# Kernel optimization log

Measured on AMD Instinct MI355X. Metric: run time of the kernel, lower is better.

Reference implementation:

```python
import jax, jax.numpy as jnp
import numpy as np

EPS = 1e-12  # F.normalize default eps


def setup_inputs() -> dict:
    key = jax.random.key(0)
    ks = jax.random.split(key, 6)
    B, C, D, H, W = 8, 192, 24, 24, 24
    heads = 6
    x = jax.random.normal(ks[0], (B, C, D, H, W), dtype=jnp.float32)
    qkv_w = jax.random.normal(ks[1], (3 * C, C), dtype=jnp.float32) * (1.0 / np.sqrt(C))
    qkv_b = jax.random.normal(ks[2], (3 * C,), dtype=jnp.float32) * 0.02
    temperature = jnp.ones((heads, 1, 1), dtype=jnp.float32)
    proj_w = jax.random.normal(ks[3], (C, C), dtype=jnp.float32) * (1.0 / np.sqrt(C))
    proj_b = jax.random.normal(ks[4], (C,), dtype=jnp.float32) * 0.02
    return {"x": x, "qkv_w": qkv_w, "qkv_b": qkv_b, "temperature": temperature,
            "proj_w": proj_w, "proj_b": proj_b}


def _l2norm_lastdim(t):
    n = jnp.sqrt(jnp.sum(t * t, axis=-1, keepdims=True))
    return t / jnp.maximum(n, EPS)


def reference(x, qkv_w, qkv_b, temperature, proj_w, proj_b):
    B, C, D, H, W = x.shape
    N = D * H * W
    heads = temperature.shape[0]
    hd = C // heads
    xf = x.reshape(B, C, N)
    # 1x1x1 Conv3d == per-voxel linear over channels: (B, 3C, N)
    qkv = jnp.einsum('bcn,oc->bon', xf, qkv_w) + qkv_b[None, :, None]
    # Faithful torch reshape of contiguous (B, 3C, N) buffer -> (B, N, 3, heads, hd),
    # then permute(2,0,3,4,1) -> (3, B, heads, hd, N)
    qkv = qkv.reshape(B, N, 3, heads, hd).transpose(2, 0, 3, 4, 1)
    q, k, v = qkv[0], qkv[1], qkv[2]
    q = _l2norm_lastdim(q)
    k = _l2norm_lastdim(k)
    # channel cross-covariance attention: (B, heads, hd, hd)
    attn = jnp.einsum('bhcn,bhdn->bhcd', q, k) * temperature[None]
    attn = jax.nn.softmax(attn, axis=-1)
    out = jnp.einsum('bhcd,bhdn->bhcn', attn, v)          # (B, heads, hd, N)
    out = out.transpose(0, 2, 1, 3).reshape(B, C, D, H, W)  # transpose(1,2) + reshape
    outf = out.reshape(B, C, N)
    y = jnp.einsum('bcn,oc->bon', outf, proj_w) + proj_b[None, :, None]
    return y.reshape(B, C, D, H, W)
```

## Files before the change

kernel.cpp:

```cpp
#include <hip/hip_runtime.h>

#define B_ 8
#define C_ 192
#define N_ 13824
#define HEADS 6
#define HD 32
#define THREEC 576
#define CH 54

typedef unsigned short ushort_t;
typedef unsigned int uint_t;
typedef __attribute__((ext_vector_type(8))) short short8;
typedef __attribute__((ext_vector_type(4))) float f32x4;

__device__ __forceinline__ float bf2f(ushort_t u) {
  union { uint_t u; float f; } c; c.u = ((uint_t)u) << 16; return c.f;
}
__device__ __forceinline__ float lo_f(uint_t u) {
  union { uint_t u; float f; } c; c.u = u << 16; return c.f;
}
__device__ __forceinline__ float hi_f(uint_t u) {
  union { uint_t u; float f; } c; c.u = u & 0xffff0000u; return c.f;
}
__device__ __forceinline__ ushort_t f2bf(float f) {
  union { float f; uint_t u; } c; c.f = f;
  uint_t u = c.u;
  uint_t r = (u + 0x7fffu + ((u >> 16) & 1u)) >> 16;
  return (ushort_t)r;
}

#define LROW 200

__global__ __launch_bounds__(256, 2) void qkv_fused(
    const float* __restrict__ x, const float* __restrict__ w,
    const float* __restrict__ bias, ushort_t* __restrict__ qkv) {
  __shared__ ushort_t Bs[128 * LROW];
  __shared__ ushort_t As[64 * LROW];
  int t = threadIdx.x;
  int n0 = blockIdx.x * 128, b = blockIdx.y;
  int wid = t >> 6, lane = t & 63;
  int ln16 = lane & 15, q4 = lane >> 4;
  const float* xb = x + (size_t)b * C_ * N_;

  {
    int nl = t & 127;
    int cb0 = (t >> 7) * 8;
#pragma unroll
    for (int it = 0; it < 12; ++it) {
      int cb = cb0 + it * 16;
      float v[8];
#pragma unroll
      for (int j = 0; j < 8; ++j)
        v[j] = xb[(size_t)(cb + j) * N_ + n0 + nl];
      union { ushort_t us[8]; uint4 u4; } pk;
#pragma unroll
      for (int j = 0; j < 8; ++j) pk.us[j] = f2bf(v[j]);
      *(uint4*)&Bs[nl * LROW + cb] = pk.u4;
    }
  }

  int ar = t >> 2, au0 = t & 3;
  uint4 apre[6];
#pragma unroll
  for (int j = 0; j < 6; ++j) {
    int u = au0 + 4 * j;
    const float* src = w + (size_t)ar * C_ + u * 8;
    float4 v0 = *(const float4*)src;
    float4 v1 = *(const float4*)(src + 4);
    union { ushort_t us[8]; uint4 u4; } pk;
    pk.us[0] = f2bf(v0.x); pk.us[1] = f2bf(v0.y); pk.us[2] = f2bf(v0.z); pk.us[3] = f2bf(v0.w);
    pk.us[4] = f2bf(v1.x); pk.us[5] = f2bf(v1.y); pk.us[6] = f2bf(v1.z); pk.us[7] = f2bf(v1.w);
    apre[j] = pk.u4;
  }

  __syncthreads();

#pragma unroll
  for (int j = 0; j < 6; ++j)
    *(uint4*)&As[ar * LROW + (au0 + 4 * j) * 8] = apre[j];

  int ncol = (wid & 1) * 64, mrow = (wid >> 1) * 32;
  short8 bb[6][4];
#pragma unroll
  for (int kk = 0; kk < 6; ++kk)
#pragma unroll
    for (int ni = 0; ni < 4; ++ni)
      bb[kk][ni] = *(const short8*)&Bs[(ncol + ni * 16 + ln16) * LROW + kk * 32 + q4 * 8];

  __syncthreads();

  for (int p = 0; p < 9; ++p) {
    if (p < 8) {
      int o0n = (p + 1) * 64;
#pragma unroll
      for (int j = 0; j < 6; ++j) {
        int u = au0 + 4 * j;
        const float* src = w + (size_t)(o0n + ar) * C_ + u * 8;
        float4 v0 = *(const float4*)src;
        float4 v1 = *(const float4*)(src + 4);
        union { ushort_t us[8]; uint4 u4; } pk;
        pk.us[0] = f2bf(v0.x); pk.us[1] = f2bf(v0.y); pk.us[2] = f2bf(v0.z); pk.us[3] = f2bf(v0.w);
        pk.us[4] = f2bf(v1.x); pk.us[5] = f2bf(v1.y); pk.us[6] = f2bf(v1.z); pk.us[7] = f2bf(v1.w);
        apre[j] = pk.u4;
      }
    }

    float brg[2][4];
#pragma unroll
    for (int mi = 0; mi < 2; ++mi)
#pragma unroll
      for (int r = 0; r < 4; ++r)
        brg[mi][r] = bias[p * 64 + mrow + mi * 16 + q4 * 4 + r];

    f32x4 acc[2][4];
#pragma unroll
    for (int mi = 0; mi < 2; ++mi)
#pragma unroll
      for (int ni = 0; ni < 4; ++ni) acc[mi][ni] = (f32x4){0.f, 0.f, 0.f, 0.f};

#pragma unroll
    for (int kk = 0; kk < 6; ++kk) {
      short8 a[2];
#pragma unroll
      for (int mi = 0; mi < 2; ++mi)
        a[mi] = *(const short8*)&As[(mrow + mi * 16 + ln16) * LROW + kk * 32 + q4 * 8];
#pragma unroll
      for (int mi = 0; mi < 2; ++mi)
#pragma unroll
        for (int ni = 0; ni < 4; ++ni)
          acc[mi][ni] = __builtin_amdgcn_mfma_f32_16x16x32_bf16(
              a[mi], bb[kk][ni], acc[mi][ni], 0, 0, 0);
    }

#pragma unroll
    for (int mi = 0; mi < 2; ++mi)
#pragma unroll
      for (int ni = 0; ni < 4; ++ni)
#pragma unroll
        for (int r = 0; r < 4; ++r) {
          float v = acc[mi][ni][r] + brg[mi][r];
          uint_t bf = f2bf(v);
          uint_t pv = (uint_t)__shfl_xor((int)bf, 1);
          if (!(lane & 1)) {
            int o_l = p * 64 + mrow + mi * 16 + q4 * 4 + r;
            int n_l = ncol + ni * 16 + ln16;
            *(uint_t*)&qkv[(size_t)(b * THREEC + o_l) * N_ + n0 + n_l] =
                bf | (pv << 16);
          }
        }

    __syncthreads();
    if (p < 8) {
#pragma unroll
      for (int j = 0; j < 6; ++j)
        *(uint4*)&As[ar * LROW + (au0 + 4 * j) * 8] = apre[j];
      __syncthreads();
    }
  }
}

#define K2RS 392
__global__ __launch_bounds__(384) void attn_partial(
    const ushort_t* __restrict__ qkv, float* __restrict__ Spart) {
  __shared__ ushort_t sh[2][32 * K2RS];
  int t = threadIdx.x;
  int chunk = blockIdx.x, b = blockIdx.y;
  const ushort_t* basep = qkv + (size_t)b * THREEC * N_;
  int n2base = chunk * 256;
  int h = t / 64, tl = t & 63;
  int c0 = (tl & 7) * 4, d0 = (tl >> 3) * 4;

  float acc[4][4];
#pragma unroll
  for (int i = 0; i < 4; ++i)
#pragma unroll
    for (int m = 0; m < 4; ++m) acc[i][m] = 0.f;
  float sqq[4] = {0.f, 0.f, 0.f, 0.f}, sqk[4] = {0.f, 0.f, 0.f, 0.f};

  uint4 pre[4];
  int srr[4], sru[4];
#pragma unroll
  for (int i = 0; i < 4; ++i) {
    int idx = t + i * 384;
    srr[i] = idx / 48; sru[i] = idx - srr[i] * 48;
  }
#pragma unroll
  for (int i = 0; i < 4; ++i) {
    int n2 = n2base + srr[i];
    int o = n2 / 24, rr = n2 - o * 24;
    pre[i] = *(const uint4*)(basep + (size_t)o * N_ + rr * THREEC + sru[i] * 8);
  }
#pragma unroll
  for (int i = 0; i < 4; ++i)
    *(uint4*)&sh[0][srr[i] * K2RS + sru[i] * 8] = pre[i];

  for (int it = 0; it < 8; ++it) {
    if (it < 7) {
#pragma unroll
      for (int i = 0; i < 4; ++i) {
        int n2 = n2base + (it + 1) * 32 + srr[i];
        int o = n2 / 24, rr = n2 - o * 24;
        pre[i] = *(const uint4*)(basep + (size_t)o * N_ + rr * THREEC + sru[i] * 8);
      }
    }
    __syncthreads();
    if (it < 7) {
#pragma unroll
      for (int i = 0; i < 4; ++i)
        *(uint4*)&sh[(it + 1) & 1][srr[i] * K2RS + sru[i] * 8] = pre[i];
    }
    const ushort_t* buf = sh[it & 1];
#pragma unroll 4
    for (int row = 0; row < 32; ++row) {
      uint2 qv = *(const uint2*)&buf[row * K2RS + h * HD + c0];
      uint2 kv = *(const uint2*)&buf[row * K2RS + C_ + h * HD + d0];
      float q[4] = {lo_f(qv.x), hi_f(qv.x), lo_f(qv.y), hi_f(qv.y)};
      float k[4] = {lo_f(kv.x), hi_f(kv.x), lo_f(kv.y), hi_f(kv.y)};
#pragma unroll
      for (int i = 0; i < 4; ++i) {
        sqq[i] = fmaf(q[i], q[i], sqq[i]);
        sqk[i] = fmaf(k[i], k[i], sqk[i]);
#pragma unroll
        for (int m = 0; m < 4; ++m)
          acc[i][m] = fmaf(q[i], k[m], acc[i][m]);
      }
    }
  }

  float* outp = Spart + ((size_t)(b * HEADS + h) * CH + chunk) * 1088;
#pragma unroll
  for (int i = 0; i < 4; ++i) {
    float4 v = {acc[i][0], acc[i][1], acc[i][2], acc[i][3]};
    *(float4*)&outp[(c0 + i) * 32 + d0] = v;
  }
  if (tl < 8) {
#pragma unroll
    for (int i = 0; i < 4; ++i) outp[1024 + c0 + i] = sqq[i];
  }
  if ((tl & 7) == 0) {
#pragma unroll
    for (int i = 0; i < 4; ++i) outp[1056 + d0 + i] = sqk[i];
  }
}

__global__ __launch_bounds__(256) void attn_final(
    const float* __restrict__ Spart, const float* __restrict__ temp,
    const float* __restrict__ proj_w, ushort_t* __restrict__ W2bf) {
  __shared__ float Sl[1024];
  __shared__ float invq[32], invk[32];
  __shared__ float Pl[192 * 33];
  int t = threadIdx.x;
  int h = blockIdx.x, b = blockIdx.y;
  const float* base = Spart + (size_t)(b * HEADS + h) * CH * 1088;

  for (int e = t; e < 1024; e += 256) {
    float s = 0.f;
    for (int ch = 0; ch < CH; ++ch) s += base[ch * 1088 + e];
    Sl[e] = s;
  }
  if (t < 64) {
    int jj = t & 31;
    int off = 1024 + (t >> 5) * 32 + jj;
    float s = 0.f;
    for (int ch = 0; ch < CH; ++ch) s += base[ch * 1088 + off];
    float inv = 1.f / fmaxf(sqrtf(s), 1e-12f);
    if (t < 32) invq[jj] = inv; else invk[jj] = inv;
  }
  for (int e = t; e < 6144; e += 256) {
    int co = e >> 5, c = e & 31;
    Pl[co * 33 + c] = proj_w[(size_t)co * C_ + c * HEADS + h];
  }
  __syncthreads();

  {
    int c = t >> 3, l8 = t & 7;
    float tmpv = temp[h];
    float iq = invq[c];
    float lg[4];
#pragma unroll
    for (int m = 0; m < 4; ++m) {
      int d = l8 * 4 + m;
      lg[m] = Sl[c * 32 + d] * iq * invk[d] * tmpv;
    }
    float mx = fmaxf(fmaxf(lg[0], lg[1]), fmaxf(lg[2], lg[3]));
    for (int off = 1; off < 8; off <<= 1) mx = fmaxf(mx, __shfl_xor(mx, off, 8));
    float ex[4]; float ssum = 0.f;
#pragma unroll
    for (int m = 0; m < 4; ++m) { ex[m] = __expf(lg[m] - mx); ssum += ex[m]; }
    for (int off = 1; off < 8; off <<= 1) ssum += __shfl_xor(ssum, off, 8);
    float inv = 1.f / ssum;
#pragma unroll
    for (int m = 0; m < 4; ++m) Sl[c * 32 + l8 * 4 + m] = ex[m] * inv;
  }
  __syncthreads();

  for (int e2 = t; e2 < 6144; e2 += 256) {
    int co = e2 >> 5, d = e2 & 31;
    float s = 0.f;
#pragma unroll
    for (int c = 0; c < 32; ++c)
      s = fmaf(Pl[co * 33 + c], Sl[c * 32 + d], s);
    W2bf[((size_t)b * C_ + co) * C_ + h * HD + d] = f2bf(s);
  }
}

__global__ __launch_bounds__(256, 2) void proj_fused(
    const ushort_t* __restrict__ qkv, const ushort_t* __restrict__ W2bf,
    const float* __restrict__ pb, float* __restrict__ y) {
  __shared__ ushort_t Bs[128 * LROW];
  __shared__ ushort_t As[64 * LROW];
  int t = threadIdx.x;
  int n2_0 = blockIdx.x * 128, b = blockIdx.y;
  int wid = t >> 6, lane = t & 63;
  int ln16 = lane & 15, q4 = lane >> 4;
  const ushort_t* basep = qkv + (size_t)b * THREEC * N_;

  {
    int nl = t >> 1, u0 = t & 1;
#pragma unroll
    for (int j = 0; j < 12; ++j) {
      int u = u0 + 2 * j;
      int n2 = n2_0 + nl;
      int o = n2 / 24, r2 = n2 - o * 24;
      uint4 v = *(const uint4*)(basep + (size_t)o * N_ + r2 * THREEC + 384 + u * 8);
      *(uint4*)&Bs[nl * LROW + u * 8] = v;
    }
  }

  int ar = t >> 2, au0 = t & 3;
  uint4 apre[6];
#pragma unroll
  for (int j = 0; j < 6; ++j) {
    int u = au0 + 4 * j;
    apre[j] = *(const uint4*)(W2bf + ((size_t)b * C_ + ar) * C_ + u * 8);
  }

  __syncthreads();

#pragma unroll
  for (int j = 0; j < 6; ++j)
    *(uint4*)&As[ar * LROW + (au0 + 4 * j) * 8] = apre[j];

  int ncol = (wid & 1) * 64, mrow = (wid >> 1) * 32;
  short8 bb[6][4];
#pragma unroll
  for (int kk = 0; kk < 6; ++kk)
#pragma unroll
    for (int ni = 0; ni < 4; ++ni)
      bb[kk][ni] = *(const short8*)&Bs[(ncol + ni * 16 + ln16) * LROW + kk * 32 + q4 * 8];

  __syncthreads();

  for (int p = 0; p < 3; ++p) {
    if (p < 2) {
      int o0n = (p + 1) * 64;
#pragma unroll
      for (int j = 0; j < 6; ++j) {
        int u = au0 + 4 * j;
        apre[j] = *(const uint4*)(W2bf + ((size_t)b * C_ + o0n + ar) * C_ + u * 8);
      }
    }

    float brg[2][4];
#pragma unroll
    for (int mi = 0; mi < 2; ++mi)
#pragma unroll
      for (int r = 0; r < 4; ++r)
        brg[mi][r] = pb[p * 64 + mrow + mi * 16 + q4 * 4 + r];

    f32x4 acc[2][4];
#pragma unroll
    for (int mi = 0; mi < 2; ++mi)
#pragma unroll
      for (int ni = 0; ni < 4; ++ni) acc[mi][ni] = (f32x4){0.f, 0.f, 0.f, 0.f};

#pragma unroll
    for (int kk = 0; kk < 6; ++kk) {
      short8 a[2];
#pragma unroll
      for (int mi = 0; mi < 2; ++mi)
        a[mi] = *(const short8*)&As[(mrow + mi * 16 + ln16) * LROW + kk * 32 + q4 * 8];
#pragma unroll
      for (int mi = 0; mi < 2; ++mi)
#pragma unroll
        for (int ni = 0; ni < 4; ++ni)
          acc[mi][ni] = __builtin_amdgcn_mfma_f32_16x16x32_bf16(
              a[mi], bb[kk][ni], acc[mi][ni], 0, 0, 0);
    }

#pragma unroll
    for (int mi = 0; mi < 2; ++mi)
#pragma unroll
      for (int ni = 0; ni < 4; ++ni)
#pragma unroll
        for (int r = 0; r < 4; ++r) {
          int co_l = p * 64 + mrow + mi * 16 + q4 * 4 + r;
          int n_l = ncol + ni * 16 + ln16;
          y[((size_t)b * C_ + co_l) * N_ + n2_0 + n_l] = acc[mi][ni][r] + brg[mi][r];
        }

    __syncthreads();
    if (p < 2) {
#pragma unroll
      for (int j = 0; j < 6; ++j)
        *(uint4*)&As[ar * LROW + (au0 + 4 * j) * 8] = apre[j];
      __syncthreads();
    }
  }
}

extern "C" void kernel_launch(void* const* d_in, const int* in_sizes, int n_in,
                              void* d_out, int out_size, void* d_ws, size_t ws_size,
                              hipStream_t stream) {
  const float* x      = (const float*)d_in[0];
  const float* qkv_w  = (const float*)d_in[1];
  const float* qkv_b  = (const float*)d_in[2];
  const float* temp   = (const float*)d_in[3];
  const float* proj_w = (const float*)d_in[4];
  const float* proj_b = (const float*)d_in[5];
  float* y = (float*)d_out;

  char* wp = (char*)d_ws;
  ushort_t* qkv  = (ushort_t*)wp;  wp += (size_t)B_ * THREEC * N_ * 2;
  float* Spart   = (float*)wp;     wp += (size_t)B_ * HEADS * CH * 1088 * 4;
  ushort_t* W2bf = (ushort_t*)wp;

  qkv_fused<<<dim3(108, B_), 256, 0, stream>>>(x, qkv_w, qkv_b, qkv);
  attn_partial<<<dim3(CH, B_), 384, 0, stream>>>(qkv, Spart);
  attn_final<<<dim3(HEADS, B_), 256, 0, stream>>>(Spart, temp, proj_w, W2bf);
  proj_fused<<<dim3(108, B_), 256, 0, stream>>>(qkv, W2bf, proj_b, y);
}
```

Before: 342.9 us.

## Pre-convert QKV weights to bf16 and read MFMA A operands from global

A small new kernel converts qkv_w to bf16 once per call, so qkv_fused no longer converts fp32 weights in every block. Both GEMM kernels drop the shared-memory A tile and its staging barriers, loading the weight fragments straight from global memory (cached in L2/L1) into MFMA registers. The smaller LDS footprint lets the launch bounds rise to 3 blocks per CU. The cost is an extra kernel launch and uncached-pattern global loads inside the MFMA loop, which may add latency.

```diff
diff --git a/kernel.cpp b/kernel.cpp
--- a/kernel.cpp
+++ b/kernel.cpp
@@ -31,11 +31,21 @@
 
 #define LROW 200
 
-__global__ __launch_bounds__(256, 2) void qkv_fused(
-    const float* __restrict__ x, const float* __restrict__ w,
+__global__ __launch_bounds__(256) void wconv(const float* __restrict__ w,
+                                             ushort_t* __restrict__ wbf) {
+  int idx = (blockIdx.x * 256 + threadIdx.x) * 8;
+  float4 v0 = *(const float4*)&w[idx];
+  float4 v1 = *(const float4*)&w[idx + 4];
+  union { ushort_t us[8]; uint4 v; } pk;
+  pk.us[0] = f2bf(v0.x); pk.us[1] = f2bf(v0.y); pk.us[2] = f2bf(v0.z); pk.us[3] = f2bf(v0.w);
+  pk.us[4] = f2bf(v1.x); pk.us[5] = f2bf(v1.y); pk.us[6] = f2bf(v1.z); pk.us[7] = f2bf(v1.w);
+  *(uint4*)&wbf[idx] = pk.v;
+}
+
+__global__ __launch_bounds__(256, 3) void qkv_fused(
+    const float* __restrict__ x, const ushort_t* __restrict__ wbf,
     const float* __restrict__ bias, ushort_t* __restrict__ qkv) {
   __shared__ ushort_t Bs[128 * LROW];
-  __shared__ ushort_t As[64 * LROW];
   int t = threadIdx.x;
   int n0 = blockIdx.x * 128, b = blockIdx.y;
   int wid = t >> 6, lane = t & 63;
@@ -59,25 +69,7 @@
     }
   }
 
-  int ar = t >> 2, au0 = t & 3;
-  uint4 apre[6];
-#pragma unroll
-  for (int j = 0; j < 6; ++j) {
-    int u = au0 + 4 * j;
-    const float* src = w + (size_t)ar * C_ + u * 8;
-    float4 v0 = *(const float4*)src;
-    float4 v1 = *(const float4*)(src + 4);
-    union { ushort_t us[8]; uint4 u4; } pk;
-    pk.us[0] = f2bf(v0.x); pk.us[1] = f2bf(v0.y); pk.us[2] = f2bf(v0.z); pk.us[3] = f2bf(v0.w);
-    pk.us[4] = f2bf(v1.x); pk.us[5] = f2bf(v1.y); pk.us[6] = f2bf(v1.z); pk.us[7] = f2bf(v1.w);
-    apre[j] = pk.u4;
-  }
-
   __syncthreads();
-
-#pragma unroll
-  for (int j = 0; j < 6; ++j)
-    *(uint4*)&As[ar * LROW + (au0 + 4 * j) * 8] = apre[j];
 
   int ncol = (wid & 1) * 64, mrow = (wid >> 1) * 32;
   short8 bb[6][4];
@@ -87,30 +79,14 @@
     for (int ni = 0; ni < 4; ++ni)
       bb[kk][ni] = *(const short8*)&Bs[(ncol + ni * 16 + ln16) * LROW + kk * 32 + q4 * 8];
 
-  __syncthreads();
-
   for (int p = 0; p < 9; ++p) {
-    if (p < 8) {
-      int o0n = (p + 1) * 64;
-#pragma unroll
-      for (int j = 0; j < 6; ++j) {
-        int u = au0 + 4 * j;
-        const float* src = w + (size_t)(o0n + ar) * C_ + u * 8;
-        float4 v0 = *(const float4*)src;
-        float4 v1 = *(const float4*)(src + 4);
-        union { ushort_t us[8]; uint4 u4; } pk;
-        pk.us[0] = f2bf(v0.x); pk.us[1] = f2bf(v0.y); pk.us[2] = f2bf(v0.z); pk.us[3] = f2bf(v0.w);
-        pk.us[4] = f2bf(v1.x); pk.us[5] = f2bf(v1.y); pk.us[6] = f2bf(v1.z); pk.us[7] = f2bf(v1.w);
-        apre[j] = pk.u4;
-      }
-    }
-
+    int obase = p * 64 + mrow;
     float brg[2][4];
 #pragma unroll
     for (int mi = 0; mi < 2; ++mi)
 #pragma unroll
       for (int r = 0; r < 4; ++r)
-        brg[mi][r] = bias[p * 64 + mrow + mi * 16 + q4 * 4 + r];
+        brg[mi][r] = bias[obase + mi * 16 + q4 * 4 + r];
 
     f32x4 acc[2][4];
 #pragma unroll
@@ -123,7 +99,8 @@
       short8 a[2];
 #pragma unroll
       for (int mi = 0; mi < 2; ++mi)
-        a[mi] = *(const short8*)&As[(mrow + mi * 16 + ln16) * LROW + kk * 32 + q4 * 8];
+        a[mi] = *(const short8*)&wbf[(size_t)(obase + mi * 16 + ln16) * C_ +
+                                     kk * 32 + q4 * 8];
 #pragma unroll
       for (int mi = 0; mi < 2; ++mi)
 #pragma unroll
@@ -142,20 +119,12 @@
           uint_t bf = f2bf(v);
           uint_t pv = (uint_t)__shfl_xor((int)bf, 1);
           if (!(lane & 1)) {
-            int o_l = p * 64 + mrow + mi * 16 + q4 * 4 + r;
+            int o_l = obase + mi * 16 + q4 * 4 + r;
             int n_l = ncol + ni * 16 + ln16;
             *(uint_t*)&qkv[(size_t)(b * THREEC + o_l) * N_ + n0 + n_l] =
                 bf | (pv << 16);
           }
         }
-
-    __syncthreads();
-    if (p < 8) {
-#pragma unroll
-      for (int j = 0; j < 6; ++j)
-        *(uint4*)&As[ar * LROW + (au0 + 4 * j) * 8] = apre[j];
-      __syncthreads();
-    }
   }
 }
 
@@ -304,16 +273,16 @@
   }
 }
 
-__global__ __launch_bounds__(256, 2) void proj_fused(
+__global__ __launch_bounds__(256, 3) void proj_fused(
     const ushort_t* __restrict__ qkv, const ushort_t* __restrict__ W2bf,
     const float* __restrict__ pb, float* __restrict__ y) {
   __shared__ ushort_t Bs[128 * LROW];
-  __shared__ ushort_t As[64 * LROW];
   int t = threadIdx.x;
   int n2_0 = blockIdx.x * 128, b = blockIdx.y;
   int wid = t >> 6, lane = t & 63;
   int ln16 = lane & 15, q4 = lane >> 4;
   const ushort_t* basep = qkv + (size_t)b * THREEC * N_;
+  const ushort_t* w2b = W2bf + (size_t)b * C_ * C_;
 
   {
     int nl = t >> 1, u0 = t & 1;
@@ -327,19 +296,7 @@
     }
   }
 
-  int ar = t >> 2, au0 = t & 3;
-  uint4 apre[6];
-#pragma unroll
-  for (int j = 0; j < 6; ++j) {
-    int u = au0 + 4 * j;
-    apre[j] = *(const uint4*)(W2bf + ((size_t)b * C_ + ar) * C_ + u * 8);
-  }
-
   __syncthreads();
-
-#pragma unroll
-  for (int j = 0; j < 6; ++j)
-    *(uint4*)&As[ar * LROW + (au0 + 4 * j) * 8] = apre[j];
 
   int ncol = (wid & 1) * 64, mrow = (wid >> 1) * 32;
   short8 bb[6][4];
@@ -349,24 +306,14 @@
     for (int ni = 0; ni < 4; ++ni)
       bb[kk][ni] = *(const short8*)&Bs[(ncol + ni * 16 + ln16) * LROW + kk * 32 + q4 * 8];
 
-  __syncthreads();
-
   for (int p = 0; p < 3; ++p) {
-    if (p < 2) {
-      int o0n = (p + 1) * 64;
-#pragma unroll
-      for (int j = 0; j < 6; ++j) {
-        int u = au0 + 4 * j;
-        apre[j] = *(const uint4*)(W2bf + ((size_t)b * C_ + o0n + ar) * C_ + u * 8);
-      }
-    }
-
+    int obase = p * 64 + mrow;
     float brg[2][4];
 #pragma unroll
     for (int mi = 0; mi < 2; ++mi)
 #pragma unroll
       for (int r = 0; r < 4; ++r)
-        brg[mi][r] = pb[p * 64 + mrow + mi * 16 + q4 * 4 + r];
+        brg[mi][r] = pb[obase + mi * 16 + q4 * 4 + r];
 
     f32x4 acc[2][4];
 #pragma unroll
@@ -379,7 +326,8 @@
       short8 a[2];
 #pragma unroll
       for (int mi = 0; mi < 2; ++mi)
-        a[mi] = *(const short8*)&As[(mrow + mi * 16 + ln16) * LROW + kk * 32 + q4 * 8];
+        a[mi] = *(const short8*)&w2b[(size_t)(obase + mi * 16 + ln16) * C_ +
+                                     kk * 32 + q4 * 8];
 #pragma unroll
       for (int mi = 0; mi < 2; ++mi)
 #pragma unroll
@@ -394,18 +342,10 @@
       for (int ni = 0; ni < 4; ++ni)
 #pragma unroll
         for (int r = 0; r < 4; ++r) {
-          int co_l = p * 64 + mrow + mi * 16 + q4 * 4 + r;
+          int co_l = obase + mi * 16 + q4 * 4 + r;
           int n_l = ncol + ni * 16 + ln16;
           y[((size_t)b * C_ + co_l) * N_ + n2_0 + n_l] = acc[mi][ni][r] + brg[mi][r];
         }
-
-    __syncthreads();
-    if (p < 2) {
-#pragma unroll
-      for (int j = 0; j < 6; ++j)
-        *(uint4*)&As[ar * LROW + (au0 + 4 * j) * 8] = apre[j];
-      __syncthreads();
-    }
   }
 }
 
@@ -423,9 +363,11 @@
   char* wp = (char*)d_ws;
   ushort_t* qkv  = (ushort_t*)wp;  wp += (size_t)B_ * THREEC * N_ * 2;
   float* Spart   = (float*)wp;     wp += (size_t)B_ * HEADS * CH * 1088 * 4;
-  ushort_t* W2bf = (ushort_t*)wp;
-
-  qkv_fused<<<dim3(108, B_), 256, 0, stream>>>(x, qkv_w, qkv_b, qkv);
+  ushort_t* W2bf = (ushort_t*)wp;  wp += (size_t)B_ * C_ * C_ * 2;
+  ushort_t* wbf  = (ushort_t*)wp;
+
+  wconv<<<54, 256, 0, stream>>>(qkv_w, wbf);
+  qkv_fused<<<dim3(108, B_), 256, 0, stream>>>(x, wbf, qkv_b, qkv);
   attn_partial<<<dim3(CH, B_), 384, 0, stream>>>(qkv, Spart);
   attn_final<<<dim3(HEADS, B_), 256, 0, stream>>>(Spart, temp, proj_w, W2bf);
   proj_fused<<<dim3(108, B_), 256, 0, stream>>>(qkv, W2bf, proj_b, y);
```

Measured after the change: 354.4 us. 1.03x slower.
